# Performance work log

Hardware: AMD Instinct MI355X
Metric: run time of the kernel (lower is better)

Reference implementation:

```python
import jax, jax.numpy as jnp
import numpy as np

B, S, H = 16, 512, 768   # batch, seq_len, bert hidden
T = 2                    # two entities per example
N, L = 32, 64            # neighbors per entity, tokens per neighbor
E = 8                    # fixed entity span length
D = 128                  # n_emb (SDPA q/k dim)
A = 128                  # a_emb (attention-attr dim)


def setup_inputs() -> dict:
    key = jax.random.key(0)
    ks = jax.random.split(key, 16)
    s = 0.02
    return {
        "xs": jax.random.normal(ks[0], (B, S, H), jnp.float32),
        "neigh_emb": jax.random.normal(ks[1], (B, T, N, L, H), jnp.float32),
        "dists": jax.random.uniform(ks[2], (B, T, N), jnp.float32) * 10.0,
        "spans": jax.random.randint(ks[3], (B, T), 0, S - E),
        "Wq": jax.random.normal(ks[4], (H, D), jnp.float32) * s,
        "bq": jnp.zeros((D,), jnp.float32),
        "Wk": jax.random.normal(ks[5], (H, D), jnp.float32) * s,
        "bk": jnp.zeros((D,), jnp.float32),
        "Wv": jax.random.normal(ks[6], (H, H), jnp.float32) * s,
        "bv": jnp.zeros((H,), jnp.float32),
        "Ww": jax.random.normal(ks[7], (H, A), jnp.float32) * s,  # w_attn_attr
        "bw": jnp.zeros((A,), jnp.float32),
        "Wa": jax.random.normal(ks[8], (2 * A, 1), jnp.float32) * s,  # attn_attr
        "ba": jnp.zeros((1,), jnp.float32),
        "wb": jax.random.normal(ks[9], (), jnp.float32) * s,  # b_attn_attr weight
        "bb": jnp.zeros((), jnp.float32),                     # b_attn_attr bias
    }


def reference(xs, neigh_emb, dists, spans, Wq, bq, Wk, bk, Wv, bv,
              Ww, bw, Wa, ba, wb, bb):
    inv_sqrt_d = 1.0 / jnp.sqrt(jnp.asarray(D, xs.dtype))
    b_idx = jnp.arange(B)[:, None, None]            # [B,1,1]
    idx = spans[:, :, None] + jnp.arange(E)         # [B,T,E] token positions

    # gather entity span features (e1_fea / e2_fea)
    e_fea = xs[b_idx, idx]                          # [B,T,E,H]

    # per-neighbor SDPA message: q from entity span, k from neighbor tokens, v = raw neighbor emb
    q = e_fea @ Wq + bq                             # [B,T,E,D]
    k = neigh_emb @ Wk + bk                         # [B,T,N,L,D]
    logits = jnp.einsum('bted,btnld->btnel', q, k) * inv_sqrt_d
    attn = jax.nn.softmax(logits, axis=-1)
    msgs = jnp.einsum('btnel,btnlh->btneh', attn, neigh_emb)  # [B,T,N,E,H]

    # custom attention score over neighbors: concat + linear + leaky + distance bias, sigmoid
    pooled = msgs.mean(axis=3)                      # [B,T,N,H]  (message.mean(1))
    feas = e_fea.mean(axis=2)                       # [B,T,H]    (e_fea.mean(dim=1))
    wf = feas @ Ww + bw                             # [B,T,A]
    wp = pooled @ Ww + bw                           # [B,T,N,A]
    cat = jnp.concatenate(
        [jnp.broadcast_to(wf[:, :, None, :], wp.shape), wp], axis=-1)  # [B,T,N,2A]
    x_att = jax.nn.leaky_relu(cat @ Wa + ba)[..., 0] + (dists * wb + bb)  # [B,T,N]
    score = jax.nn.sigmoid(x_att)                   # attn_type='sigmoid'

    # attention-weighted scatter-add of messages back into entity token spans
    delta = jnp.einsum('btn,btneh->bteh', score, msgs)
    x = xs.at[b_idx, idx].add(delta)                # [B,S,H]

    # final full self-attention over updated sequence
    q2 = x @ Wq + bq                                # [B,S,D]
    k2 = x @ Wk + bk                                # [B,S,D]
    v2 = x @ Wv + bv                                # [B,S,H]
    s2 = jnp.einsum('bsd,bmd->bsm', q2, k2) * inv_sqrt_d
    out = jnp.einsum('bsm,bmh->bsh', jax.nn.softmax(s2, axis=-1), v2)
    return out
```

## Files before the change

kernel.cpp:

```cpp
#include <hip/hip_runtime.h>
#include <hip/hip_bf16.h>

constexpr int B = 16, S = 512, H = 768, T = 2, N = 32, L = 64, E = 8, D = 128, A = 128;
constexpr float INV_SQRT_D = 0.08838834764831843f;

__device__ __forceinline__ void gemm128(const float* __restrict__ Ap, int lda,
                                        const float* __restrict__ W, int ldw,
                                        const float* __restrict__ bias,
                                        float* __restrict__ C, int ldc,
                                        int r0, int c0, int K) {
    __shared__ float As[32][132];
    __shared__ float Ws[32][128];
    const int tid = threadIdx.x;
    const int tr = (tid >> 4) << 3;
    const int tc = (tid & 15) << 3;
    float acc[8][8];
    #pragma unroll
    for (int i = 0; i < 8; i++)
        #pragma unroll
        for (int j = 0; j < 8; j++) acc[i][j] = 0.f;

    const int ar = tid >> 3;
    const int ak = (tid & 7) << 2;
    const int wr = tid >> 5;
    const int wc = (tid & 31) << 2;

    for (int k0 = 0; k0 < K; k0 += 32) {
        float4 av[4], wv[4];
        #pragma unroll
        for (int p = 0; p < 4; p++) {
            av[p] = *(const float4*)&Ap[(size_t)(r0 + ar + 32 * p) * lda + k0 + ak];
            wv[p] = *(const float4*)&W[(size_t)(k0 + wr + 8 * p) * ldw + c0 + wc];
        }
        __syncthreads();
        #pragma unroll
        for (int p = 0; p < 4; p++) {
            As[ak + 0][ar + 32 * p] = av[p].x;
            As[ak + 1][ar + 32 * p] = av[p].y;
            As[ak + 2][ar + 32 * p] = av[p].z;
            As[ak + 3][ar + 32 * p] = av[p].w;
            *(float4*)&Ws[wr + 8 * p][wc] = wv[p];
        }
        __syncthreads();
        #pragma unroll
        for (int kk = 0; kk < 32; kk++) {
            float a[8], b[8];
            *(float4*)&a[0] = *(const float4*)&As[kk][tr];
            *(float4*)&a[4] = *(const float4*)&As[kk][tr + 4];
            *(float4*)&b[0] = *(const float4*)&Ws[kk][tc];
            *(float4*)&b[4] = *(const float4*)&Ws[kk][tc + 4];
            #pragma unroll
            for (int i = 0; i < 8; i++)
                #pragma unroll
                for (int j = 0; j < 8; j++) acc[i][j] += a[i] * b[j];
        }
    }
    #pragma unroll
    for (int i = 0; i < 8; i++) {
        float o[8];
        #pragma unroll
        for (int j = 0; j < 8; j++)
            o[j] = acc[i][j] + (bias ? bias[c0 + tc + j] : 0.f);
        *(float4*)&C[(size_t)(r0 + tr + i) * ldc + c0 + tc] = *(float4*)&o[0];
        *(float4*)&C[(size_t)(r0 + tr + i) * ldc + c0 + tc + 4] = *(float4*)&o[4];
    }
}

__global__ void k_qk2(const float* __restrict__ x,
                      const float* __restrict__ Wq, const float* __restrict__ bq,
                      const float* __restrict__ Wk, const float* __restrict__ bk,
                      float* __restrict__ q2, float* __restrict__ k2) {
    const float* W = blockIdx.y ? Wk : Wq;
    const float* bs = blockIdx.y ? bk : bq;
    float* C = blockIdx.y ? k2 : q2;
    gemm128(x, H, W, D, bs, C, D, blockIdx.x * 128, 0, H);
}

__global__ void k_pv(const float* __restrict__ P, const float* __restrict__ v2,
                     float* __restrict__ out) {
    int b = blockIdx.z;
    gemm128(P + (size_t)b * S * S, S, v2 + (size_t)b * S * H, H, nullptr,
            out + (size_t)b * S * H, H, blockIdx.x * 128, blockIdx.y * 128, S);
}

__global__ void k_qkT(const float* __restrict__ q2, const float* __restrict__ k2,
                      float* __restrict__ Smat) {
    __shared__ float Qs[32][132];
    __shared__ float Ks[32][132];
    const int b = blockIdx.z;
    const int r0 = blockIdx.x * 128, c0 = blockIdx.y * 128;
    const float* Qb = q2 + (size_t)b * S * D;
    const float* Kb = k2 + (size_t)b * S * D;
    float* Sb = Smat + (size_t)b * S * S;
    const int tid = threadIdx.x;
    const int tr = (tid >> 4) << 3;
    const int tc = (tid & 15) << 3;
    const int ar = tid >> 3;
    const int ak = (tid & 7) << 2;
    float acc[8][8];
    #pragma unroll
    for (int i = 0; i < 8; i++)
        #pragma unroll
        for (int j = 0; j < 8; j++) acc[i][j] = 0.f;

    for (int k0 = 0; k0 < D; k0 += 32) {
        float4 qv[4], kv[4];
        #pragma unroll
        for (int p = 0; p < 4; p++) {
            qv[p] = *(const float4*)&Qb[(size_t)(r0 + ar + 32 * p) * D + k0 + ak];
            kv[p] = *(const float4*)&Kb[(size_t)(c0 + ar + 32 * p) * D + k0 + ak];
        }
        __syncthreads();
        #pragma unroll
        for (int p = 0; p < 4; p++) {
            Qs[ak + 0][ar + 32 * p] = qv[p].x;
            Qs[ak + 1][ar + 32 * p] = qv[p].y;
            Qs[ak + 2][ar + 32 * p] = qv[p].z;
            Qs[ak + 3][ar + 32 * p] = qv[p].w;
            Ks[ak + 0][ar + 32 * p] = kv[p].x;
            Ks[ak + 1][ar + 32 * p] = kv[p].y;
            Ks[ak + 2][ar + 32 * p] = kv[p].z;
            Ks[ak + 3][ar + 32 * p] = kv[p].w;
        }
        __syncthreads();
        #pragma unroll
        for (int kk = 0; kk < 32; kk++) {
            float a[8], bb_[8];
            *(float4*)&a[0] = *(const float4*)&Qs[kk][tr];
            *(float4*)&a[4] = *(const float4*)&Qs[kk][tr + 4];
            *(float4*)&bb_[0] = *(const float4*)&Ks[kk][tc];
            *(float4*)&bb_[4] = *(const float4*)&Ks[kk][tc + 4];
            #pragma unroll
            for (int i = 0; i < 8; i++)
                #pragma unroll
                for (int j = 0; j < 8; j++) acc[i][j] += a[i] * bb_[j];
        }
    }
    #pragma unroll
    for (int i = 0; i < 8; i++) {
        float o[8];
        #pragma unroll
        for (int j = 0; j < 8; j++) o[j] = acc[i][j] * INV_SQRT_D;
        *(float4*)&Sb[(size_t)(r0 + tr + i) * S + c0 + tc] = *(float4*)&o[0];
        *(float4*)&Sb[(size_t)(r0 + tr + i) * S + c0 + tc + 4] = *(float4*)&o[4];
    }
}

__global__ void k_smax(float* __restrict__ Smat) {
    int row = blockIdx.x * 4 + (threadIdx.x >> 6);
    int lane = threadIdx.x & 63;
    float* p = Smat + (size_t)row * S;
    float4 v0 = *(const float4*)&p[lane * 4];
    float4 v1 = *(const float4*)&p[256 + lane * 4];
    float m = fmaxf(fmaxf(fmaxf(v0.x, v0.y), fmaxf(v0.z, v0.w)),
                    fmaxf(fmaxf(v1.x, v1.y), fmaxf(v1.z, v1.w)));
    #pragma unroll
    for (int off = 32; off; off >>= 1) m = fmaxf(m, __shfl_xor(m, off, 64));
    v0.x = expf(v0.x - m); v0.y = expf(v0.y - m);
    v0.z = expf(v0.z - m); v0.w = expf(v0.w - m);
    v1.x = expf(v1.x - m); v1.y = expf(v1.y - m);
    v1.z = expf(v1.z - m); v1.w = expf(v1.w - m);
    float s = v0.x + v0.y + v0.z + v0.w + v1.x + v1.y + v1.z + v1.w;
    #pragma unroll
    for (int off = 32; off; off >>= 1) s += __shfl_xor(s, off, 64);
    float inv = 1.0f / s;
    v0.x *= inv; v0.y *= inv; v0.z *= inv; v0.w *= inv;
    v1.x *= inv; v1.y *= inv; v1.z *= inv; v1.w *= inv;
    *(float4*)&p[lane * 4] = v0;
    *(float4*)&p[256 + lane * 4] = v1;
}

__global__ void k_gather(const float* __restrict__ xs,
                         const int* __restrict__ spans,
                         float* __restrict__ e_fea, float* __restrict__ feas) {
    int bt = blockIdx.x;
    int b = bt / T;
    int span = spans[bt];
    for (int h = threadIdx.x; h < H; h += 256) {
        float acc = 0.f;
        for (int e = 0; e < E; e++) {
            float v = xs[((size_t)b * S + span + e) * H + h];
            e_fea[((size_t)bt * E + e) * H + h] = v;
            acc += v;
        }
        feas[(size_t)bt * H + h] = acc * (1.0f / E);
    }
}

__global__ void k_qproj(const float* __restrict__ e_fea,
                        const float* __restrict__ Wq,
                        const float* __restrict__ bq,
                        float* __restrict__ q) {
    int row = blockIdx.x;
    int d = threadIdx.x;
    const float* er = e_fea + (size_t)row * H;
    float acc = bq[d];
    #pragma unroll 4
    for (int h = 0; h < H; h++) acc += er[h] * Wq[(size_t)h * D + d];
    q[(size_t)row * D + d] = acc;
}

__global__ void k_qkw(const float* __restrict__ q, const float* __restrict__ Wk,
                      const float* __restrict__ bk,
                      float* __restrict__ qkb, float* __restrict__ qb0) {
    __shared__ float q_s[E * D];
    const int bt = blockIdx.x;
    const float* qp = q + (size_t)bt * E * D;
    for (int i = threadIdx.x; i < E * D; i += 256) q_s[i] = qp[i];
    __syncthreads();
    const int h = blockIdx.y * 256 + threadIdx.x;
    float acc[E];
    #pragma unroll
    for (int e = 0; e < E; e++) acc[e] = 0.f;
    const float* wrow = Wk + (size_t)h * D;
    for (int d = 0; d < D; d += 4) {
        float4 wv = *(const float4*)&wrow[d];
        #pragma unroll
        for (int e = 0; e < E; e++) {
            float4 qv = *(const float4*)&q_s[e * D + d];
            acc[e] += qv.x * wv.x + qv.y * wv.y + qv.z * wv.z + qv.w * wv.w;
        }
    }
    #pragma unroll
    for (int e = 0; e < E; e++)
        qkb[((size_t)bt * E + e) * H + h] = acc[e];
    if (blockIdx.y == 0 && threadIdx.x < E) {
        int e = threadIdx.x;
        float s = 0.f;
        for (int d = 0; d < D; d++) s += q_s[e * D + d] * bk[d];
        qb0[bt * E + e] = s;
    }
}

__global__ void k_sdpa(const float* __restrict__ qkb, const float* __restrict__ qb0,
                       const float* __restrict__ neigh,
                       float* __restrict__ attn_p, float* __restrict__ pooled) {
    __shared__ float qk_s[E * H];
    __shared__ float u_s[64 * 69];
    __shared__ float attn_s[E * L];
    __shared__ float abar_s[L];
    __shared__ float qb0_s[E];
    const int btn = blockIdx.x;
    const int bt = btn >> 5;
    const float* qkp = qkb + (size_t)bt * E * H;
    const float* nrow = neigh + (size_t)btn * L * H;
    const int tid = threadIdx.x;
    const int l = tid & 63;
    const int g = tid >> 6;

    for (int i = tid; i < E * H / 4; i += 256)
        *(float4*)&qk_s[i * 4] = *(const float4*)&qkp[i * 4];
    if (tid < E) qb0_s[tid] = qb0[bt * E + tid];

    float acc[E];
    #pragma unroll
    for (int e = 0; e < E; e++) acc[e] = 0.f;

    for (int c = 0; c < H / 64; c++) {
        const int h0 = c * 64;
        __syncthreads();
        for (int i = tid; i < 64 * 64; i += 256) {
            int ll = i >> 6, hh = i & 63;
            u_s[ll * 69 + hh] = nrow[(size_t)ll * H + h0 + hh];
        }
        __syncthreads();
        const int hb = g * 16;
        #pragma unroll
        for (int h = 0; h < 16; h += 4) {
            float n0 = u_s[l * 69 + hb + h + 0];
            float n1 = u_s[l * 69 + hb + h + 1];
            float n2 = u_s[l * 69 + hb + h + 2];
            float n3 = u_s[l * 69 + hb + h + 3];
            #pragma unroll
            for (int e = 0; e < E; e++) {
                float4 qv = *(const float4*)&qk_s[e * H + h0 + hb + h];
                acc[e] += qv.x * n0 + qv.y * n1 + qv.z * n2 + qv.w * n3;
            }
        }
    }
    __syncthreads();
    float* red = u_s;
    *(float4*)&red[g * 512 + l * 8 + 0] = make_float4(acc[0], acc[1], acc[2], acc[3]);
    *(float4*)&red[g * 512 + l * 8 + 4] = make_float4(acc[4], acc[5], acc[6], acc[7]);
    __syncthreads();
    for (int p = tid; p < E * L; p += 256) {
        int e = p >> 6, ll = p & 63;
        float s = red[ll * 8 + e] + red[512 + ll * 8 + e] +
                  red[1024 + ll * 8 + e] + red[1536 + ll * 8 + e];
        attn_s[e * L + ll] = (s + qb0_s[e]) * INV_SQRT_D;
    }
    __syncthreads();

    if (tid < E) {
        int e = tid;
        float m = -1e30f;
        for (int ll = 0; ll < L; ll++) m = fmaxf(m, attn_s[e * L + ll]);
        float ssum = 0.f;
        for (int ll = 0; ll < L; ll++) {
            float ex = expf(attn_s[e * L + ll] - m);
            attn_s[e * L + ll] = ex;
            ssum += ex;
        }
        float inv = 1.0f / ssum;
        for (int ll = 0; ll < L; ll++) attn_s[e * L + ll] *= inv;
    }
    __syncthreads();

    for (int i = tid; i < E * L; i += 256)
        attn_p[(size_t)btn * E * L + i] = attn_s[i];
    if (tid < L) {
        float s = 0.f;
        #pragma unroll
        for (int e = 0; e < E; e++) s += attn_s[e * L + tid];
        abar_s[tid] = s * (1.0f / E);
    }
    __syncthreads();

    for (int h = tid; h < H; h += 256) {
        float acc2 = 0.f;
        for (int ll = 0; ll < L; ll++) acc2 += abar_s[ll] * nrow[(size_t)ll * H + h];
        pooled[(size_t)btn * H + h] = acc2;
    }
}

__global__ void k_uv(const float* __restrict__ Ww, const float* __restrict__ bw,
                     const float* __restrict__ Wa, const float* __restrict__ ba,
                     const float* __restrict__ wb, const float* __restrict__ bb,
                     float* __restrict__ misc) {
    int h = blockIdx.x * blockDim.x + threadIdx.x;
    if (h < H) {
        float lo = 0.f, hi = 0.f;
        for (int a = 0; a < A; a++) {
            float w = Ww[(size_t)h * A + a];
            lo += w * Wa[a];
            hi += w * Wa[A + a];
        }
        misc[h] = lo;
        misc[H + h] = hi;
    }
    if (blockIdx.x == 0 && threadIdx.x == 0) {
        float c = ba[0];
        for (int a = 0; a < A; a++) c += bw[a] * (Wa[a] + Wa[A + a]);
        misc[2 * H] = c;
        misc[2 * H + 1] = wb[0];
        misc[2 * H + 2] = bb[0];
    }
}

__global__ void k_score(const float* __restrict__ feas, const float* __restrict__ pooled,
                        const float* __restrict__ misc, const float* __restrict__ dists,
                        float* __restrict__ score) {
    __shared__ float red[4];
    int btn = blockIdx.x;
    int bt = btn / N;
    float part = 0.f;
    for (int h = threadIdx.x; h < H; h += 256)
        part += feas[(size_t)bt * H + h] * misc[h] + pooled[(size_t)btn * H + h] * misc[H + h];
    #pragma unroll
    for (int off = 32; off > 0; off >>= 1) part += __shfl_down(part, off, 64);
    if ((threadIdx.x & 63) == 0) red[threadIdx.x >> 6] = part;
    __syncthreads();
    if (threadIdx.x == 0) {
        float tot = red[0] + red[1] + red[2] + red[3] + misc[2 * H];
        float lk = tot > 0.f ? tot : 0.01f * tot;
        float xatt = lk + dists[btn] * misc[2 * H + 1] + misc[2 * H + 2];
        score[btn] = 1.0f / (1.0f + expf(-xatt));
    }
}

__global__ void k_delta(const float* __restrict__ attn_p, const float* __restrict__ score,
                        const float* __restrict__ neigh, float* __restrict__ delta) {
    __shared__ float w_s[E * 8];
    int bt = blockIdx.x, l0 = blockIdx.y * 8;
    float acc[E][3];
    #pragma unroll
    for (int e = 0; e < E; e++)
        #pragma unroll
        for (int c = 0; c < 3; c++) acc[e][c] = 0.f;
    for (int n = 0; n < N; n++) {
        int btn = bt * N + n;
        if (threadIdx.x < E * 8) {
            int e = threadIdx.x >> 3, lp = threadIdx.x & 7;
            w_s[threadIdx.x] = score[btn] * attn_p[((size_t)btn * E + e) * L + l0 + lp];
        }
        __syncthreads();
        const float* nrow = neigh + ((size_t)btn * L + l0) * H;
        for (int lp = 0; lp < 8; lp++) {
            float nv[3];
            #pragma unroll
            for (int c = 0; c < 3; c++) nv[c] = nrow[(size_t)lp * H + threadIdx.x + c * 256];
            #pragma unroll
            for (int e = 0; e < E; e++) {
                float w = w_s[e * 8 + lp];
                #pragma unroll
                for (int c = 0; c < 3; c++) acc[e][c] += w * nv[c];
            }
        }
        __syncthreads();
    }
    #pragma unroll
    for (int e = 0; e < E; e++)
        #pragma unroll
        for (int c = 0; c < 3; c++)
            atomicAdd(&delta[((size_t)bt * E + e) * H + threadIdx.x + c * 256], acc[e][c]);
}

__global__ void k_addspan(const float* __restrict__ delta, const int* __restrict__ spans,
                          float* __restrict__ x) {
    int i = blockIdx.x * 256 + threadIdx.x;
    int h = i % H;
    int e = (i / H) % E;
    int bt = i / (H * E);
    int b = bt / T;
    atomicAdd(&x[((size_t)b * S + spans[bt] + e) * H + h], delta[i]);
}

__global__ __launch_bounds__(256, 3) void k_v2(float* __restrict__ xv,
                                               const float* __restrict__ Wv,
                                               const float* __restrict__ bv) {
    __shared__ float x_s[H][16];
    const int r0 = blockIdx.x * 16;
    const int t = threadIdx.x;

    {
        const int r = t & 15;
        const int h0 = (t >> 4) * 48;
        const float* xp = &xv[(size_t)(r0 + r) * H + h0];
        #pragma unroll
        for (int j = 0; j < 48; j += 4) {
            float4 v = *(const float4*)&xp[j];
            x_s[h0 + j + 0][r] = v.x;
            x_s[h0 + j + 1][r] = v.y;
            x_s[h0 + j + 2][r] = v.z;
            x_s[h0 + j + 3][r] = v.w;
        }
    }
    __syncthreads();

    float acc[3][16];
    #pragma unroll
    for (int c = 0; c < 3; c++)
        #pragma unroll
        for (int r = 0; r < 16; r++) acc[c][r] = 0.f;

    const float* wp = Wv + t;
    for (int h = 0; h < H; h += 4) {
        float w[4][3];
        #pragma unroll
        for (int u = 0; u < 4; u++) {
            const float* wr = wp + (size_t)(h + u) * H;
            w[u][0] = wr[0];
            w[u][1] = wr[256];
            w[u][2] = wr[512];
        }
        #pragma unroll
        for (int u = 0; u < 4; u++) {
            float xr[16];
            *(float4*)&xr[0]  = *(const float4*)&x_s[h + u][0];
            *(float4*)&xr[4]  = *(const float4*)&x_s[h + u][4];
            *(float4*)&xr[8]  = *(const float4*)&x_s[h + u][8];
            *(float4*)&xr[12] = *(const float4*)&x_s[h + u][12];
            #pragma unroll
            for (int c = 0; c < 3; c++)
                #pragma unroll
                for (int r = 0; r < 16; r++)
                    acc[c][r] += xr[r] * w[u][c];
        }
    }
    #pragma unroll
    for (int c = 0; c < 3; c++) {
        const float bias = bv[c * 256 + t];
        #pragma unroll
        for (int r = 0; r < 16; r++)
            xv[(size_t)(r0 + r) * H + c * 256 + t] = acc[c][r] + bias;
    }
}

extern "C" void kernel_launch(void* const* d_in, const int* in_sizes, int n_in,
                              void* d_out, int out_size, void* d_ws, size_t ws_size,
                              hipStream_t stream) {
    const float* xs    = (const float*)d_in[0];
    const float* neigh = (const float*)d_in[1];
    const float* dists = (const float*)d_in[2];
    const int*   spans = (const int*)d_in[3];
    const float* Wq = (const float*)d_in[4];
    const float* bq = (const float*)d_in[5];
    const float* Wk = (const float*)d_in[6];
    const float* bk = (const float*)d_in[7];
    const float* Wv = (const float*)d_in[8];
    const float* bv = (const float*)d_in[9];
    const float* Ww = (const float*)d_in[10];
    const float* bw = (const float*)d_in[11];
    const float* Wa = (const float*)d_in[12];
    const float* ba = (const float*)d_in[13];
    const float* wb = (const float*)d_in[14];
    const float* bb = (const float*)d_in[15];
    float* out = (float*)d_out;

    float* ws     = (float*)d_ws;
    float* regB   = ws + (size_t)8388608;
    float* attn_p = regB;
    float* pooled = attn_p + (size_t)B * T * N * E * L;
    float* delta  = pooled + (size_t)B * T * N * H;
    float* e_fea  = delta + (size_t)B * T * E * H;
    float* qb     = e_fea + (size_t)B * T * E * H;
    float* feas   = qb + (size_t)B * T * E * D;
    float* misc   = feas + (size_t)B * T * H;
    float* scoreb = misc + 2048;
    float* qkb    = scoreb + 1024;
    float* qb0b   = qkb + (size_t)B * T * E * H;
    float* x      = ws;
    float* q2     = ws + (size_t)B * S * H;
    float* k2     = q2 + (size_t)B * S * D;
    float* v2     = x;
    float* Smat   = regB;

    k_gather<<<B * T, 256, 0, stream>>>(xs, spans, e_fea, feas);
    k_qproj<<<B * T * E, D, 0, stream>>>(e_fea, Wq, bq, qb);
    k_qkw<<<dim3(B * T, 3), 256, 0, stream>>>(qb, Wk, bk, qkb, qb0b);
    k_sdpa<<<B * T * N, 256, 0, stream>>>(qkb, qb0b, neigh, attn_p, pooled);
    k_uv<<<3, 256, 0, stream>>>(Ww, bw, Wa, ba, wb, bb, misc);
    k_score<<<B * T * N, 256, 0, stream>>>(feas, pooled, misc, dists, scoreb);
    hipMemsetAsync(delta, 0, (size_t)B * T * E * H * sizeof(float), stream);
    k_delta<<<dim3(B * T, L / 8), 256, 0, stream>>>(attn_p, scoreb, neigh, delta);
    hipMemcpyAsync(x, xs, (size_t)B * S * H * sizeof(float), hipMemcpyDeviceToDevice, stream);
    k_addspan<<<(B * T * E * H) / 256, 256, 0, stream>>>(delta, spans, x);
    k_qk2<<<dim3(B * S / 128, 2), 256, 0, stream>>>(x, Wq, bq, Wk, bk, q2, k2);
    k_v2<<<B * S / 16, 256, 0, stream>>>(v2, Wv, bv);
    k_qkT<<<dim3(S / 128, S / 128, B), 256, 0, stream>>>(q2, k2, Smat);
    k_smax<<<B * S / 4, 256, 0, stream>>>(Smat);
    k_pv<<<dim3(S / 128, H / 128, B), 256, 0, stream>>>(Smat, v2, out);
}
```

Measured before the change: 1.011 ms.

## Fuse score computation into SDPA kernel via per-token projected dot products

Instead of materializing pooled neighbor vectors and running a separate score kernel, the SDPA kernel now accumulates each neighbor token's dot product with the Ww·Wa projection while streaming the tile, then combines it with mean attention weights to produce the sigmoid score directly. The entity-feature term is precomputed in k_qkw. It also register-prefetches the next neighbor tile during the SDPA loop and sets launch bounds. This removes a second full pass over neigh_emb and the pooled buffer, at the cost of extra registers and shared memory in k_sdpa.

```diff
diff --git a/kernel.cpp b/kernel.cpp
--- a/kernel.cpp
+++ b/kernel.cpp
@@ -202,8 +202,11 @@
 
 __global__ void k_qkw(const float* __restrict__ q, const float* __restrict__ Wk,
                       const float* __restrict__ bk,
-                      float* __restrict__ qkb, float* __restrict__ qb0) {
+                      const float* __restrict__ feas, const float* __restrict__ misc,
+                      float* __restrict__ qkb, float* __restrict__ qb0,
+                      float* __restrict__ feasv) {
     __shared__ float q_s[E * D];
+    __shared__ float redf[4];
     const int bt = blockIdx.x;
     const float* qp = q + (size_t)bt * E * D;
     for (int i = threadIdx.x; i < E * D; i += 256) q_s[i] = qp[i];
@@ -224,21 +227,34 @@
     #pragma unroll
     for (int e = 0; e < E; e++)
         qkb[((size_t)bt * E + e) * H + h] = acc[e];
-    if (blockIdx.y == 0 && threadIdx.x < E) {
-        int e = threadIdx.x;
-        float s = 0.f;
-        for (int d = 0; d < D; d++) s += q_s[e * D + d] * bk[d];
-        qb0[bt * E + e] = s;
-    }
-}
-
-__global__ void k_sdpa(const float* __restrict__ qkb, const float* __restrict__ qb0,
-                       const float* __restrict__ neigh,
-                       float* __restrict__ attn_p, float* __restrict__ pooled) {
+    if (blockIdx.y == 0) {
+        if (threadIdx.x < E) {
+            int e = threadIdx.x;
+            float s = 0.f;
+            for (int d = 0; d < D; d++) s += q_s[e * D + d] * bk[d];
+            qb0[bt * E + e] = s;
+        }
+        float part = 0.f;
+        for (int hh = threadIdx.x; hh < H; hh += 256)
+            part += feas[(size_t)bt * H + hh] * misc[hh];
+        #pragma unroll
+        for (int off = 32; off > 0; off >>= 1) part += __shfl_down(part, off, 64);
+        if ((threadIdx.x & 63) == 0) redf[threadIdx.x >> 6] = part;
+        __syncthreads();
+        if (threadIdx.x == 0)
+            feasv[bt] = redf[0] + redf[1] + redf[2] + redf[3];
+    }
+}
+
+__global__ __launch_bounds__(256, 3) void k_sdpa(
+        const float* __restrict__ qkb, const float* __restrict__ qb0,
+        const float* __restrict__ neigh, const float* __restrict__ misc,
+        const float* __restrict__ feasv, const float* __restrict__ dists,
+        float* __restrict__ attn_p, float* __restrict__ score) {
     __shared__ float qk_s[E * H];
     __shared__ float u_s[64 * 69];
+    __shared__ float uvec[H];
     __shared__ float attn_s[E * L];
-    __shared__ float abar_s[L];
     __shared__ float qb0_s[E];
     const int btn = blockIdx.x;
     const int bt = btn >> 5;
@@ -247,24 +263,43 @@
     const int tid = threadIdx.x;
     const int l = tid & 63;
     const int g = tid >> 6;
+    const int hb = g * 16;
 
     for (int i = tid; i < E * H / 4; i += 256)
         *(float4*)&qk_s[i * 4] = *(const float4*)&qkp[i * 4];
+    for (int i = tid; i < H / 4; i += 256)
+        *(float4*)&uvec[i * 4] = *(const float4*)&misc[H + i * 4];
     if (tid < E) qb0_s[tid] = qb0[bt * E + tid];
 
     float acc[E];
     #pragma unroll
     for (int e = 0; e < E; e++) acc[e] = 0.f;
+    float nu = 0.f;
+
+    const int pll = tid >> 4;
+    const int ph4 = (tid & 15) * 4;
+    float4 pr[4];
+    #pragma unroll
+    for (int j = 0; j < 4; j++)
+        pr[j] = *(const float4*)&nrow[(size_t)(j * 16 + pll) * H + ph4];
 
     for (int c = 0; c < H / 64; c++) {
         const int h0 = c * 64;
         __syncthreads();
-        for (int i = tid; i < 64 * 64; i += 256) {
-            int ll = i >> 6, hh = i & 63;
-            u_s[ll * 69 + hh] = nrow[(size_t)ll * H + h0 + hh];
-        }
-        __syncthreads();
-        const int hb = g * 16;
+        #pragma unroll
+        for (int j = 0; j < 4; j++) {
+            const int base = (j * 16 + pll) * 69 + ph4;
+            u_s[base + 0] = pr[j].x;
+            u_s[base + 1] = pr[j].y;
+            u_s[base + 2] = pr[j].z;
+            u_s[base + 3] = pr[j].w;
+        }
+        if (c + 1 < H / 64) {
+            #pragma unroll
+            for (int j = 0; j < 4; j++)
+                pr[j] = *(const float4*)&nrow[(size_t)(j * 16 + pll) * H + h0 + 64 + ph4];
+        }
+        __syncthreads();
         #pragma unroll
         for (int h = 0; h < 16; h += 4) {
             float n0 = u_s[l * 69 + hb + h + 0];
@@ -276,12 +311,16 @@
                 float4 qv = *(const float4*)&qk_s[e * H + h0 + hb + h];
                 acc[e] += qv.x * n0 + qv.y * n1 + qv.z * n2 + qv.w * n3;
             }
+            float4 uq = *(const float4*)&uvec[h0 + hb + h];
+            nu += n0 * uq.x + n1 * uq.y + n2 * uq.z + n3 * uq.w;
         }
     }
     __syncthreads();
     float* red = u_s;
+    float* nured = u_s + 2048;
     *(float4*)&red[g * 512 + l * 8 + 0] = make_float4(acc[0], acc[1], acc[2], acc[3]);
     *(float4*)&red[g * 512 + l * 8 + 4] = make_float4(acc[4], acc[5], acc[6], acc[7]);
+    nured[g * 64 + l] = nu;
     __syncthreads();
     for (int p = tid; p < E * L; p += 256) {
         int e = p >> 6, ll = p & 63;
@@ -308,18 +347,22 @@
 
     for (int i = tid; i < E * L; i += 256)
         attn_p[(size_t)btn * E * L + i] = attn_s[i];
-    if (tid < L) {
-        float s = 0.f;
-        #pragma unroll
-        for (int e = 0; e < E; e++) s += attn_s[e * L + tid];
-        abar_s[tid] = s * (1.0f / E);
-    }
-    __syncthreads();
-
-    for (int h = tid; h < H; h += 256) {
-        float acc2 = 0.f;
-        for (int ll = 0; ll < L; ll++) acc2 += abar_s[ll] * nrow[(size_t)ll * H + h];
-        pooled[(size_t)btn * H + h] = acc2;
+
+    if (tid < 64) {
+        float a = 0.f;
+        #pragma unroll
+        for (int e = 0; e < E; e++) a += attn_s[e * L + tid];
+        a *= (1.0f / E);
+        float nl = nured[tid] + nured[64 + tid] + nured[128 + tid] + nured[192 + tid];
+        float part = a * nl;
+        #pragma unroll
+        for (int off = 32; off > 0; off >>= 1) part += __shfl_xor(part, off, 64);
+        if (tid == 0) {
+            float tot = feasv[bt] + part + misc[2 * H];
+            float lk = tot > 0.f ? tot : 0.01f * tot;
+            float xatt = lk + dists[btn] * misc[2 * H + 1] + misc[2 * H + 2];
+            score[btn] = 1.0f / (1.0f + expf(-xatt));
+        }
     }
 }
 
@@ -344,27 +387,6 @@
         misc[2 * H] = c;
         misc[2 * H + 1] = wb[0];
         misc[2 * H + 2] = bb[0];
-    }
-}
-
-__global__ void k_score(const float* __restrict__ feas, const float* __restrict__ pooled,
-                        const float* __restrict__ misc, const float* __restrict__ dists,
-                        float* __restrict__ score) {
-    __shared__ float red[4];
-    int btn = blockIdx.x;
-    int bt = btn / N;
-    float part = 0.f;
-    for (int h = threadIdx.x; h < H; h += 256)
-        part += feas[(size_t)bt * H + h] * misc[h] + pooled[(size_t)btn * H + h] * misc[H + h];
-    #pragma unroll
-    for (int off = 32; off > 0; off >>= 1) part += __shfl_down(part, off, 64);
-    if ((threadIdx.x & 63) == 0) red[threadIdx.x >> 6] = part;
-    __syncthreads();
-    if (threadIdx.x == 0) {
-        float tot = red[0] + red[1] + red[2] + red[3] + misc[2 * H];
-        float lk = tot > 0.f ? tot : 0.01f * tot;
-        float xatt = lk + dists[btn] * misc[2 * H + 1] + misc[2 * H + 2];
-        score[btn] = 1.0f / (1.0f + expf(-xatt));
     }
 }
 
@@ -500,8 +522,7 @@
     float* ws     = (float*)d_ws;
     float* regB   = ws + (size_t)8388608;
     float* attn_p = regB;
-    float* pooled = attn_p + (size_t)B * T * N * E * L;
-    float* delta  = pooled + (size_t)B * T * N * H;
+    float* delta  = attn_p + (size_t)B * T * N * E * L;
     float* e_fea  = delta + (size_t)B * T * E * H;
     float* qb     = e_fea + (size_t)B * T * E * H;
     float* feas   = qb + (size_t)B * T * E * D;
@@ -509,6 +530,7 @@
     float* scoreb = misc + 2048;
     float* qkb    = scoreb + 1024;
     float* qb0b   = qkb + (size_t)B * T * E * H;
+    float* feasvb = qb0b + 256;
     float* x      = ws;
     float* q2     = ws + (size_t)B * S * H;
     float* k2     = q2 + (size_t)B * S * D;
@@ -516,11 +538,11 @@
     float* Smat   = regB;
 
     k_gather<<<B * T, 256, 0, stream>>>(xs, spans, e_fea, feas);
+    k_uv<<<3, 256, 0, stream>>>(Ww, bw, Wa, ba, wb, bb, misc);
     k_qproj<<<B * T * E, D, 0, stream>>>(e_fea, Wq, bq, qb);
-    k_qkw<<<dim3(B * T, 3), 256, 0, stream>>>(qb, Wk, bk, qkb, qb0b);
-    k_sdpa<<<B * T * N, 256, 0, stream>>>(qkb, qb0b, neigh, attn_p, pooled);
-    k_uv<<<3, 256, 0, stream>>>(Ww, bw, Wa, ba, wb, bb, misc);
-    k_score<<<B * T * N, 256, 0, stream>>>(feas, pooled, misc, dists, scoreb);
+    k_qkw<<<dim3(B * T, 3), 256, 0, stream>>>(qb, Wk, bk, feas, misc, qkb, qb0b, feasvb);
+    k_sdpa<<<B * T * N, 256, 0, stream>>>(qkb, qb0b, neigh, misc, feasvb, dists,
+                                          attn_p, scoreb);
     hipMemsetAsync(delta, 0, (size_t)B * T * E * H * sizeof(float), stream);
     k_delta<<<dim3(B * T, L / 8), 256, 0, stream>>>(attn_p, scoreb, neigh, delta);
     hipMemcpyAsync(x, xs, (size_t)B * S * H * sizeof(float), hipMemcpyDeviceToDevice, stream);
```

Result: faster. 903.8 us (-10.6%).
